# Kernel tuning notes

Hardware: AMD Instinct MI355X
Metric: run time of the kernel (lower is better)

The kernel has to match this reference:

```python
import jax, jax.numpy as jnp
import numpy as np

N = 100_000      # points
F = 64           # feature dim
B = 4            # graphs in batch
POOL_RAD = 0.2   # voxel size
D = 8            # static upper bound on voxels per spatial dim
M_MAX = 1024     # static upper bound on number of nonempty clusters


def setup_inputs() -> dict:
    key = jax.random.key(0)
    k1, k2, k3 = jax.random.split(key, 3)
    pos = jax.random.uniform(k1, (N, 3), dtype=jnp.float32)
    x = jax.random.normal(k2, (N, F), dtype=jnp.float32)
    batch = jnp.sort(jax.random.randint(k3, (N,), 0, B)).astype(jnp.int32)
    return {"pos": pos, "x": x, "batch": batch}


def reference(pos, x, batch):
    batch = batch.astype(jnp.int32)
    rad = jnp.asarray(POOL_RAD, pos.dtype)
    # --- voxel_grid clustering (start = min - rad/2 as in the torch module) ---
    start = pos.min(axis=0) - rad * 0.5
    coords = jnp.clip(jnp.floor((pos - start) / rad).astype(jnp.int32), 0, D - 1)  # [N,3]
    vox = ((batch * D + coords[:, 0]) * D + coords[:, 1]) * D + coords[:, 2]       # [N]
    V = B * D * D * D
    # --- consecutive_cluster + scatter mean of positions ---
    ones = jnp.ones((pos.shape[0],), pos.dtype)
    counts = jax.ops.segment_sum(ones, vox, num_segments=V)       # [V]
    sum_pos = jax.ops.segment_sum(pos, vox, num_segments=V)       # [V,3]
    nonempty = counts > 0
    # compact nonempty voxels to static M_MAX slots (padding duplicates voxel idx 0;
    # argmin tie-breaking to the first index keeps duplicates inert)
    idx = jnp.nonzero(nonempty, size=M_MAX, fill_value=0)[0]      # [M_MAX]
    valid = jnp.arange(M_MAX) < jnp.sum(nonempty)                 # [M_MAX]
    centroids = sum_pos[idx] / jnp.maximum(counts[idx], 1.0)[:, None]  # [M_MAX,3]
    new_batch = idx // (D * D * D)                                # [M_MAX]
    # --- nearest: assign each point to nearest cluster centroid in same graph ---
    d2 = (jnp.sum(pos * pos, axis=1)[:, None]
          - 2.0 * pos @ centroids.T
          + jnp.sum(centroids * centroids, axis=1)[None, :])      # [N, M_MAX]
    big = jnp.asarray(1e30, pos.dtype)
    d2 = jnp.where((batch[:, None] == new_batch[None, :]) & valid[None, :], d2, big)
    assign = jnp.argmin(d2, axis=1)                               # [N]
    # --- scatter max of features into clusters (empty clusters -> 0, as in PyG) ---
    x_pool = jax.ops.segment_max(x, assign, num_segments=M_MAX)   # [M_MAX, F]
    x_pool = jnp.where(jnp.isfinite(x_pool), x_pool, jnp.zeros_like(x_pool))
    return x_pool, centroids, new_batch, valid
```

## Files before the change

kernel.cpp:

```cpp
#include <hip/hip_runtime.h>
#include <stdint.h>

#define DGRID 8
#define NVOX  2048
#define NBATCH 4
#define MMAX  1024
#define FDIM  64
#define CHUNKP 256
#define GRP   20

__device__ __forceinline__ unsigned encf(float f){
  unsigned u = __float_as_uint(f);
  return (u & 0x80000000u) ? ~u : (u | 0x80000000u);
}
__device__ __forceinline__ float decf(unsigned e){
  unsigned u = (e & 0x80000000u) ? (e ^ 0x80000000u) : ~e;
  return __uint_as_float(u);
}


__global__ __launch_bounds__(256) void k_minpart(const float* __restrict__ pos,
    int N, unsigned* __restrict__ bmin){
  unsigned m0 = 0xFFFFFFFFu, m1 = 0xFFFFFFFFu, m2 = 0xFFFFFFFFu;
  int stride = gridDim.x * blockDim.x;
  for (int i = blockIdx.x * blockDim.x + threadIdx.x; i < N; i += stride){
    unsigned e0 = encf(pos[3*i+0]); if (e0 < m0) m0 = e0;
    unsigned e1 = encf(pos[3*i+1]); if (e1 < m1) m1 = e1;
    unsigned e2 = encf(pos[3*i+2]); if (e2 < m2) m2 = e2;
  }
  #pragma unroll
  for (int off = 32; off > 0; off >>= 1){
    unsigned t0 = __shfl_down(m0, off); if (t0 < m0) m0 = t0;
    unsigned t1 = __shfl_down(m1, off); if (t1 < m1) m1 = t1;
    unsigned t2 = __shfl_down(m2, off); if (t2 < m2) m2 = t2;
  }
  __shared__ unsigned sm[4][3];
  int wv = threadIdx.x >> 6, lane = threadIdx.x & 63;
  if (lane == 0){ sm[wv][0] = m0; sm[wv][1] = m1; sm[wv][2] = m2; }
  __syncthreads();
  if (threadIdx.x == 0){
    unsigned a0 = sm[0][0], a1 = sm[0][1], a2 = sm[0][2];
    for (int k = 1; k < 4; k++){
      if (sm[k][0] < a0) a0 = sm[k][0];
      if (sm[k][1] < a1) a1 = sm[k][1];
      if (sm[k][2] < a2) a2 = sm[k][2];
    }
    bmin[blockIdx.x*3+0] = a0;
    bmin[blockIdx.x*3+1] = a1;
    bmin[blockIdx.x*3+2] = a2;
  }
}

__global__ __launch_bounds__(256) void k_vox_hist(const float* __restrict__ pos,
    const int* __restrict__ batch, int N, const unsigned* __restrict__ bmin,
    int* __restrict__ vox, int* __restrict__ chunkHist){
  __shared__ int h[NVOX];
  __shared__ unsigned smin[3];
  for (int t = threadIdx.x; t < NVOX; t += 256) h[t] = 0;
  if (threadIdx.x < 64){
    unsigned a0 = bmin[threadIdx.x*3+0];
    unsigned a1 = bmin[threadIdx.x*3+1];
    unsigned a2 = bmin[threadIdx.x*3+2];
    #pragma unroll
    for (int off = 32; off > 0; off >>= 1){
      unsigned t0 = __shfl_down(a0, off); if (t0 < a0) a0 = t0;
      unsigned t1 = __shfl_down(a1, off); if (t1 < a1) a1 = t1;
      unsigned t2 = __shfl_down(a2, off); if (t2 < a2) a2 = t2;
    }
    if (threadIdx.x == 0){ smin[0] = a0; smin[1] = a1; smin[2] = a2; }
  }
  __syncthreads();
  int c = blockIdx.x;
  int i = c * CHUNKP + threadIdx.x;
  if (i < N){
    float s0 = __fsub_rn(decf(smin[0]), 0.1f);
    float s1 = __fsub_rn(decf(smin[1]), 0.1f);
    float s2 = __fsub_rn(decf(smin[2]), 0.1f);
    float q0 = __fdiv_rn(__fsub_rn(pos[3*i+0], s0), 0.2f);
    float q1 = __fdiv_rn(__fsub_rn(pos[3*i+1], s1), 0.2f);
    float q2 = __fdiv_rn(__fsub_rn(pos[3*i+2], s2), 0.2f);
    int c0 = (int)floorf(q0); c0 = c0 < 0 ? 0 : (c0 > DGRID-1 ? DGRID-1 : c0);
    int c1 = (int)floorf(q1); c1 = c1 < 0 ? 0 : (c1 > DGRID-1 ? DGRID-1 : c1);
    int c2 = (int)floorf(q2); c2 = c2 < 0 ? 0 : (c2 > DGRID-1 ? DGRID-1 : c2);
    int v = ((batch[i]*DGRID + c0)*DGRID + c1)*DGRID + c2;
    vox[i] = v;
    atomicAdd(&h[v], 1);
  }
  __syncthreads();
  for (int t = threadIdx.x; t < NVOX; t += 256)
    chunkHist[c * NVOX + t] = h[t];
}

__global__ __launch_bounds__(256) void k_gsum(int nchunks, int ngroups,
    const int* __restrict__ chunkHist, int* __restrict__ gsum){
  int g = blockIdx.x >> 3;
  int v = (blockIdx.x & 7) * 256 + threadIdx.x;
  if (g >= ngroups) return;
  int c0 = g * GRP, c1 = min(nchunks, c0 + GRP);
  int s = 0;
  for (int c = c0; c < c1; c++) s += chunkHist[c * NVOX + v];
  gsum[g * NVOX + v] = s;
}

__global__ __launch_bounds__(256) void k_gscan(int ngroups,
    int* __restrict__ gsum, int* __restrict__ counts, int* __restrict__ clustCnt){
  if (blockIdx.x < 4) clustCnt[blockIdx.x * 256 + threadIdx.x] = 0;
  int v = blockIdx.x * 256 + threadIdx.x;
  if (v >= NVOX) return;
  int run = 0;
  for (int g = 0; g < ngroups; g++){
    int t = gsum[g * NVOX + v];
    gsum[g * NVOX + v] = run;
    run += t;
  }
  counts[v] = run;
}

__global__ __launch_bounds__(64) void k_scan_fast(const int* __restrict__ counts,
    int* Mout, int* batchStartC, int* __restrict__ idxOfCluster,
    int* __restrict__ voxBase){
  int lane = threadIdx.x;
  int cs[32];
  int ne = 0, tot = 0;
  #pragma unroll
  for (int j = 0; j < 32; j++){
    int c = counts[lane*32 + j];
    cs[j] = c;
    ne += (c > 0) ? 1 : 0;
    tot += c;
  }
  int inc = ne, incT = tot;
  #pragma unroll
  for (int off = 1; off < 64; off <<= 1){
    int t  = __shfl_up(inc,  off);
    int tt = __shfl_up(incT, off);
    if (lane >= off){ inc += t; incT += tt; }
  }
  int exne = inc - ne;
  int bb   = incT - tot;
  int run = exne;
  #pragma unroll
  for (int j = 0; j < 32; j++){
    voxBase[lane*32 + j] = bb;
    bb += cs[j];
    if (cs[j] > 0){
      if (run < MMAX) idxOfCluster[run] = lane*32 + j;
      run++;
    }
  }
  int M = __shfl(run, 63);
  for (int m = M + lane; m < MMAX; m += 64) idxOfCluster[m] = 0;
  int ex0  = __shfl(exne, 0);
  int ex16 = __shfl(exne, 16);
  int ex32 = __shfl(exne, 32);
  int ex48 = __shfl(exne, 48);
  if (lane == 0){
    Mout[0] = M;
    batchStartC[0] = ex0;  batchStartC[1] = ex16;
    batchStartC[2] = ex32; batchStartC[3] = ex48;
    batchStartC[NBATCH] = (M < MMAX) ? M : MMAX;
  }
}

__global__ __launch_bounds__(256) void k_scatter(const float* __restrict__ pos,
    const int* __restrict__ vox, int N, const int* __restrict__ chunkHist,
    const int* __restrict__ gsum, const int* __restrict__ voxBase,
    float* __restrict__ pos_sorted){
  __shared__ int base[NVOX];
  __shared__ int rowCnt[4][NVOX];
  int c = blockIdx.x;
  int g = c / GRP, cg0 = g * GRP;
  for (int t = threadIdx.x; t < NVOX; t += 256){
    int b = voxBase[t] + gsum[g * NVOX + t];
    for (int cc = cg0; cc < c; cc++) b += chunkHist[cc * NVOX + t];
    base[t] = b;
    rowCnt[0][t] = 0; rowCnt[1][t] = 0; rowCnt[2][t] = 0; rowCnt[3][t] = 0;
  }
  __syncthreads();
  int r = threadIdx.x >> 6;
  int lane = threadIdx.x & 63;
  int i = c * CHUNKP + r*64 + lane;
  bool valid = i < N;
  int v = valid ? vox[i] : -1;
  float px = 0.f, py = 0.f, pz = 0.f;
  if (valid){ px = pos[3*i+0]; py = pos[3*i+1]; pz = pos[3*i+2]; }
  int rank = 0, cnt = 0;
  #pragma unroll 8
  for (int j = 0; j < 64; j++){
    int vj = __shfl(v, j);
    if (vj == v){
      cnt++;
      if (j < lane) rank++;
    }
  }
  if (valid && rank == 0) rowCnt[r][v] = cnt;
  __syncthreads();
  if (valid){
    int pre = 0;
    for (int rr = 0; rr < r; rr++) pre += rowCnt[rr][v];
    int dst = base[v] + pre + rank;
    pos_sorted[3*dst+0] = px;
    pos_sorted[3*dst+1] = py;
    pos_sorted[3*dst+2] = pz;
  }
}

__global__ __launch_bounds__(64) void k_sum2cent(const float* __restrict__ pos_sorted,
    const int* __restrict__ voxBase, const int* __restrict__ counts,
    float4* __restrict__ centv){
  int v = blockIdx.x * 64 + threadIdx.x;
  if (v >= NVOX) return;
  int lo = voxBase[v], cnt = counts[v];
  const float* p = pos_sorted + 3*(size_t)lo;
  float sx = 0.f, sy = 0.f, sz = 0.f;
  int k = 0;
  for (; k + 4 <= cnt; k += 4){
    float a0 = p[0],  a1 = p[1],  a2 = p[2];
    float b0 = p[3],  b1 = p[4],  b2 = p[5];
    float c0 = p[6],  c1 = p[7],  c2 = p[8];
    float d0 = p[9],  d1 = p[10], d2 = p[11];
    sx = __fadd_rn(__fadd_rn(__fadd_rn(__fadd_rn(sx, a0), b0), c0), d0);
    sy = __fadd_rn(__fadd_rn(__fadd_rn(__fadd_rn(sy, a1), b1), c1), d1);
    sz = __fadd_rn(__fadd_rn(__fadd_rn(__fadd_rn(sz, a2), b2), c2), d2);
    p += 12;
  }
  for (; k < cnt; k++){
    sx = __fadd_rn(sx, p[0]);
    sy = __fadd_rn(sy, p[1]);
    sz = __fadd_rn(sz, p[2]);
    p += 3;
  }
  float den = fmaxf((float)cnt, 1.0f);
  float cx = __fdiv_rn(sx, den);
  float cy = __fdiv_rn(sy, den);
  float cz = __fdiv_rn(sz, den);
  float c2 = __fadd_rn(__fadd_rn(__fmul_rn(cx,cx), __fmul_rn(cy,cy)), __fmul_rn(cz,cz));
  centv[v] = make_float4(cx, cy, cz, c2);
}

__global__ __launch_bounds__(256) void k_argmin2(const float* __restrict__ pos,
    const int* __restrict__ batch, int N, const float4* __restrict__ centv,
    const int* __restrict__ idxOfCluster, const int* __restrict__ Mout,
    const int* __restrict__ batchStartC, int* __restrict__ assign,
    int* __restrict__ clustCnt, float* __restrict__ outC,
    float* __restrict__ outNB, float* __restrict__ outValid){
  __shared__ float4 sc[MMAX];
  __shared__ int h[MMAX];
  for (int m = threadIdx.x; m < MMAX; m += 256){
    sc[m] = centv[idxOfCluster[m]];
    h[m] = 0;
  }
  __syncthreads();
  if (blockIdx.x == 0){
    int M = Mout[0];
    for (int m = threadIdx.x; m < MMAX; m += 256){
      float4 cc = sc[m];
      outC[3*m+0] = cc.x; outC[3*m+1] = cc.y; outC[3*m+2] = cc.z;
      outNB[m] = (float)(idxOfCluster[m] >> 9);
      outValid[m] = (m < M) ? 1.0f : 0.0f;
    }
  }
  int i = blockIdx.x * 256 + threadIdx.x;
  if (i < N){
    float px = pos[3*i+0], py = pos[3*i+1], pz = pos[3*i+2];
    float p2 = __fadd_rn(__fadd_rn(__fmul_rn(px,px), __fmul_rn(py,py)), __fmul_rn(pz,pz));
    int b = batch[i];
    int mlo = batchStartC[b], mhi = batchStartC[b+1];
    float best = 3.402823466e+38f;
    int bm = mlo;
    for (int m = mlo; m < mhi; m++){
      float4 cc = sc[m];
      float dot = __fadd_rn(__fadd_rn(__fmul_rn(px,cc.x), __fmul_rn(py,cc.y)),
                            __fmul_rn(pz,cc.z));
      float d2  = __fadd_rn(__fsub_rn(p2, __fmul_rn(2.0f, dot)), cc.w);
      if (d2 < best){ best = d2; bm = m; }
    }
    assign[i] = bm;
    atomicAdd(&h[bm], 1);
  }
  __syncthreads();
  for (int t = threadIdx.x; t < MMAX; t += 256){
    int c = h[t];
    if (c > 0) atomicAdd(&clustCnt[t], c);
  }
}

__global__ __launch_bounds__(64) void k_cbase2(const int* __restrict__ clustCnt,
    int* __restrict__ clustBase, int* __restrict__ cur){
  int lane = threadIdx.x;
  int cs[16]; int tot = 0;
  #pragma unroll
  for (int j = 0; j < 16; j++){ cs[j] = clustCnt[lane*16 + j]; tot += cs[j]; }
  int inc = tot;
  #pragma unroll
  for (int off = 1; off < 64; off <<= 1){
    int t = __shfl_up(inc, off);
    if (lane >= off) inc += t;
  }
  int bb = inc - tot;
  #pragma unroll
  for (int j = 0; j < 16; j++){
    clustBase[lane*16 + j] = bb;
    cur[lane*16 + j] = bb;
    bb += cs[j];
  }
}

__global__ __launch_bounds__(256) void k_scatter2s(const int* __restrict__ assign,
    int N, int* __restrict__ cur, int* __restrict__ idx_sorted){
  int i = blockIdx.x * 256 + threadIdx.x;
  if (i >= N) return;
  int m = assign[i];
  int p = atomicAdd(&cur[m], 1);
  idx_sorted[p] = i;
}

__global__ __launch_bounds__(256) void k_xmax(const float* __restrict__ x,
    const int* __restrict__ idx_sorted, const int* __restrict__ clustBase,
    const int* __restrict__ clustCnt, float* __restrict__ outX){
  int w = blockIdx.x * 4 + (threadIdx.x >> 6);
  int lane = threadIdx.x & 63;
  if (w >= MMAX) return;
  int lo = clustBase[w], cnt = clustCnt[w];
  float mx = -3.402823466e+38f;
  int k = 0;
  for (; k + 4 <= cnt; k += 4){
    int r0 = idx_sorted[lo+k+0], r1 = idx_sorted[lo+k+1];
    int r2 = idx_sorted[lo+k+2], r3 = idx_sorted[lo+k+3];
    float a = x[(size_t)r0 * FDIM + lane];
    float b = x[(size_t)r1 * FDIM + lane];
    float c = x[(size_t)r2 * FDIM + lane];
    float d = x[(size_t)r3 * FDIM + lane];
    mx = fmaxf(mx, fmaxf(fmaxf(a, b), fmaxf(c, d)));
  }
  for (; k < cnt; k++){
    int r0 = idx_sorted[lo+k];
    mx = fmaxf(mx, x[(size_t)r0 * FDIM + lane]);
  }
  outX[w * FDIM + lane] = (cnt > 0) ? mx : 0.0f;
}


__global__ __launch_bounds__(256) void k_init(unsigned* startEnc, int* batchCnt){
  int t = threadIdx.x;
  if (t < 3) startEnc[t] = 0xFFFFFFFFu;
  if (t < NBATCH) batchCnt[t] = 0;
}

__global__ __launch_bounds__(256) void k_min_hist(const float* __restrict__ pos,
    const int* __restrict__ batch, int N, unsigned* startEnc, int* batchCnt){
  __shared__ int sbin[NBATCH];
  if (threadIdx.x < NBATCH) sbin[threadIdx.x] = 0;
  __syncthreads();
  unsigned m0 = 0xFFFFFFFFu, m1 = 0xFFFFFFFFu, m2 = 0xFFFFFFFFu;
  int stride = gridDim.x * blockDim.x;
  for (int i = blockIdx.x * blockDim.x + threadIdx.x; i < N; i += stride){
    unsigned e0 = encf(pos[3*i+0]); if (e0 < m0) m0 = e0;
    unsigned e1 = encf(pos[3*i+1]); if (e1 < m1) m1 = e1;
    unsigned e2 = encf(pos[3*i+2]); if (e2 < m2) m2 = e2;
    atomicAdd(&sbin[batch[i]], 1);
  }
  #pragma unroll
  for (int off = 32; off > 0; off >>= 1){
    unsigned t0 = __shfl_down(m0, off); if (t0 < m0) m0 = t0;
    unsigned t1 = __shfl_down(m1, off); if (t1 < m1) m1 = t1;
    unsigned t2 = __shfl_down(m2, off); if (t2 < m2) m2 = t2;
  }
  if ((threadIdx.x & 63) == 0){
    atomicMin(&startEnc[0], m0);
    atomicMin(&startEnc[1], m1);
    atomicMin(&startEnc[2], m2);
  }
  __syncthreads();
  if (threadIdx.x < NBATCH) atomicAdd(&batchCnt[threadIdx.x], sbin[threadIdx.x]);
}

__global__ __launch_bounds__(256) void k_vox(const float* __restrict__ pos,
    const int* __restrict__ batch, int N, const unsigned* __restrict__ startEnc,
    int* __restrict__ vox, int* __restrict__ counts){
  int i = blockIdx.x * blockDim.x + threadIdx.x;
  if (i >= N) return;
  float s0 = __fsub_rn(decf(startEnc[0]), 0.1f);
  float s1 = __fsub_rn(decf(startEnc[1]), 0.1f);
  float s2 = __fsub_rn(decf(startEnc[2]), 0.1f);
  float q0 = __fdiv_rn(__fsub_rn(pos[3*i+0], s0), 0.2f);
  float q1 = __fdiv_rn(__fsub_rn(pos[3*i+1], s1), 0.2f);
  float q2 = __fdiv_rn(__fsub_rn(pos[3*i+2], s2), 0.2f);
  int c0 = (int)floorf(q0); c0 = c0 < 0 ? 0 : (c0 > DGRID-1 ? DGRID-1 : c0);
  int c1 = (int)floorf(q1); c1 = c1 < 0 ? 0 : (c1 > DGRID-1 ? DGRID-1 : c1);
  int c2 = (int)floorf(q2); c2 = c2 < 0 ? 0 : (c2 > DGRID-1 ? DGRID-1 : c2);
  int v = ((batch[i]*DGRID + c0)*DGRID + c1)*DGRID + c2;
  vox[i] = v;
  atomicAdd(&counts[v], 1);
}

__global__ __launch_bounds__(64) void k_scan_old(const int* __restrict__ counts,
    const int* __restrict__ batchCnt, int* batchPtr, int* Mout,
    int* batchStartC, int* __restrict__ idxOfCluster, int* __restrict__ voxBase){
  int lane = threadIdx.x;
  int cs[32];
  int ne = 0, tot = 0;
  #pragma unroll
  for (int j = 0; j < 32; j++){
    int c = counts[lane*32 + j];
    cs[j] = c;
    ne += (c > 0) ? 1 : 0;
    tot += c;
  }
  int inc = ne, incT = tot;
  #pragma unroll
  for (int off = 1; off < 64; off <<= 1){
    int t  = __shfl_up(inc,  off);
    int tt = __shfl_up(incT, off);
    if (lane >= off){ inc += t; incT += tt; }
  }
  int exne = inc - ne;
  int bb   = incT - tot;
  int run = exne;
  #pragma unroll
  for (int j = 0; j < 32; j++){
    voxBase[lane*32 + j] = bb;
    bb += cs[j];
    if (cs[j] > 0){
      if (run < MMAX) idxOfCluster[run] = lane*32 + j;
      run++;
    }
  }
  int M = __shfl(run, 63);
  for (int m = M + lane; m < MMAX; m += 64) idxOfCluster[m] = 0;
  int ex0  = __shfl(exne, 0);
  int ex16 = __shfl(exne, 16);
  int ex32 = __shfl(exne, 32);
  int ex48 = __shfl(exne, 48);
  if (lane == 0){
    Mout[0] = M;
    int acc = 0;
    for (int b = 0; b < NBATCH; b++){ batchPtr[b] = acc; acc += batchCnt[b]; }
    batchPtr[NBATCH] = acc;
    batchStartC[0] = ex0;  batchStartC[1] = ex16;
    batchStartC[2] = ex32; batchStartC[3] = ex48;
    batchStartC[NBATCH] = (M < MMAX) ? M : MMAX;
  }
}

__global__ __launch_bounds__(64) void k_sum(const float* __restrict__ pos,
    const int* __restrict__ vox, const int* __restrict__ counts,
    const int* __restrict__ batchPtr, float* __restrict__ sum_pos){
  int v = blockIdx.x * 64 + threadIdx.x;
  if (v >= NVOX) return;
  int b = v >> 9;
  int lo = batchPtr[b], hi = batchPtr[b+1];
  float sx = 0.f, sy = 0.f, sz = 0.f;
  if (counts[v] > 0){
    for (int i = lo; i < hi; i++){
      if (vox[i] == v){
        sx = __fadd_rn(sx, pos[3*i+0]);
        sy = __fadd_rn(sy, pos[3*i+1]);
        sz = __fadd_rn(sz, pos[3*i+2]);
      }
    }
  }
  sum_pos[3*v+0] = sx;
  sum_pos[3*v+1] = sy;
  sum_pos[3*v+2] = sz;
}

__global__ __launch_bounds__(256) void k_cent(const float* __restrict__ sum_pos,
    const int* __restrict__ counts, const int* __restrict__ idxOfCluster,
    const int* __restrict__ Mout, float4* __restrict__ cent4,
    float* __restrict__ outC, float* __restrict__ outNB, float* __restrict__ outValid){
  int m = blockIdx.x * blockDim.x + threadIdx.x;
  if (m >= MMAX) return;
  int M = Mout[0];
  int v = idxOfCluster[m];
  float den = fmaxf((float)counts[v], 1.0f);
  float cx = __fdiv_rn(sum_pos[3*v+0], den);
  float cy = __fdiv_rn(sum_pos[3*v+1], den);
  float cz = __fdiv_rn(sum_pos[3*v+2], den);
  float c2 = __fadd_rn(__fadd_rn(__fmul_rn(cx,cx), __fmul_rn(cy,cy)), __fmul_rn(cz,cz));
  cent4[m] = make_float4(cx, cy, cz, c2);
  outC[3*m+0] = cx; outC[3*m+1] = cy; outC[3*m+2] = cz;
  outNB[m] = (float)(v >> 9);
  outValid[m] = (m < M) ? 1.0f : 0.0f;
}

__global__ __launch_bounds__(256) void k_assign_slow(const float* __restrict__ pos,
    const float* __restrict__ x, const int* __restrict__ batch, int N,
    const float4* __restrict__ cent4, const int* __restrict__ batchStartC,
    unsigned* __restrict__ encMax){
  __shared__ float4 sc[MMAX];
  for (int m = threadIdx.x; m < MMAX; m += blockDim.x) sc[m] = cent4[m];
  __syncthreads();
  int i = blockIdx.x * blockDim.x + threadIdx.x;
  if (i >= N) return;
  float px = pos[3*i+0], py = pos[3*i+1], pz = pos[3*i+2];
  float p2 = __fadd_rn(__fadd_rn(__fmul_rn(px,px), __fmul_rn(py,py)), __fmul_rn(pz,pz));
  int b = batch[i];
  int mlo = batchStartC[b], mhi = batchStartC[b+1];
  float best = 3.402823466e+38f;
  int bm = mlo;
  for (int m = mlo; m < mhi; m++){
    float4 c = sc[m];
    float dot = __fadd_rn(__fadd_rn(__fmul_rn(px,c.x), __fmul_rn(py,c.y)),
                          __fmul_rn(pz,c.z));
    float d2  = __fadd_rn(__fsub_rn(p2, __fmul_rn(2.0f, dot)), c.w);
    if (d2 < best){ best = d2; bm = m; }
  }
  unsigned* dst = encMax + bm * FDIM;
  const float4* xi = (const float4*)(x + (size_t)i * FDIM);
  #pragma unroll
  for (int f4 = 0; f4 < FDIM/4; f4++){
    float4 xv = xi[f4];
    atomicMax(&dst[4*f4+0], encf(xv.x));
    atomicMax(&dst[4*f4+1], encf(xv.y));
    atomicMax(&dst[4*f4+2], encf(xv.z));
    atomicMax(&dst[4*f4+3], encf(xv.w));
  }
}
__global__ __launch_bounds__(256) void k_decode(const unsigned* __restrict__ encMax,
    float* __restrict__ outX){
  int t = blockIdx.x * blockDim.x + threadIdx.x;
  if (t >= MMAX * FDIM) return;
  unsigned e = encMax[t];
  outX[t] = (e == 0u) ? 0.0f : decf(e);
}


extern "C" void kernel_launch(void* const* d_in, const int* in_sizes, int n_in,
                              void* d_out, int out_size, void* d_ws, size_t ws_size,
                              hipStream_t stream){
  const float* pos   = (const float*)d_in[0];
  const float* x     = (const float*)d_in[1];
  const int*   batch = (const int*)d_in[2];
  const int N = in_sizes[2];

  char* w = (char*)d_ws;
  unsigned* bmin         = (unsigned*)(w + 0);
  unsigned* startEnc     = (unsigned*)(w + 768);
  int*      batchCnt     = (int*)(w + 784);
  int*      batchPtr     = (int*)(w + 800);
  int*      Mout         = (int*)(w + 832);
  int*      batchStartC  = (int*)(w + 848);
  int*      counts       = (int*)(w + 896);
  int*      voxBase      = (int*)(w + 9088);
  float*    sum_pos      = (float*)(w + 17280);
  int*      idxOfCluster = (int*)(w + 41856);
  float4*   cent4        = (float4*)(w + 45952);
  int*      clustCnt     = (int*)(w + 62336);
  int*      clustBase    = (int*)(w + 66432);
  int*      cur          = (int*)(w + 70528);
  float4*   centv        = (float4*)(w + 74624);
  unsigned* encMax       = (unsigned*)(w + 107392);
  int*      gsum         = (int*)(w + 107392);
  int*      vox          = (int*)(w + 369536);
  size_t voxEnd = 369536 + (size_t)N * 4;
  size_t chOff  = (voxEnd + 15) & ~(size_t)15;

  int nchunks = (N + CHUNKP - 1) / CHUNKP;
  int ngroups = (nchunks + GRP - 1) / GRP;
  size_t psOff = chOff + (size_t)nchunks * NVOX * 4;
  size_t need  = psOff + (size_t)N * 3 * 4;
  const bool fast = (ws_size >= need) && (ngroups <= 32);

  int*   chunkHist  = (int*)(w + chOff);
  float* pos_sorted = (float*)(w + psOff);
  int* assign     = (int*)pos_sorted;
  int* idx_sorted = (int*)pos_sorted + N;

  float* outX     = (float*)d_out;
  float* outC     = outX + MMAX * FDIM;
  float* outNB    = outC + MMAX * 3;
  float* outValid = outNB + MMAX;

  const int nb = (N + 255) / 256;
  if (fast){
    k_minpart<<<64, 256, 0, stream>>>(pos, N, bmin);
    k_vox_hist<<<nchunks, 256, 0, stream>>>(pos, batch, N, bmin, vox, chunkHist);
    k_gsum<<<ngroups * 8, 256, 0, stream>>>(nchunks, ngroups, chunkHist, gsum);
    k_gscan<<<NVOX / 256, 256, 0, stream>>>(ngroups, gsum, counts, clustCnt);
    k_scan_fast<<<1, 64, 0, stream>>>(counts, Mout, batchStartC, idxOfCluster, voxBase);
    k_scatter<<<nchunks, 256, 0, stream>>>(pos, vox, N, chunkHist, gsum, voxBase,
                                           pos_sorted);
    k_sum2cent<<<NVOX / 64, 64, 0, stream>>>(pos_sorted, voxBase, counts, centv);
    k_argmin2<<<nb, 256, 0, stream>>>(pos, batch, N, centv, idxOfCluster, Mout,
                                      batchStartC, assign, clustCnt,
                                      outC, outNB, outValid);
    k_cbase2<<<1, 64, 0, stream>>>(clustCnt, clustBase, cur);
    k_scatter2s<<<nb, 256, 0, stream>>>(assign, N, cur, idx_sorted);
    k_xmax<<<MMAX / 4, 256, 0, stream>>>(x, idx_sorted, clustBase, clustCnt, outX);
  } else {
    k_init<<<1, 256, 0, stream>>>(startEnc, batchCnt);
    hipMemsetAsync(counts, 0, NVOX * 4, stream);
    hipMemsetAsync(encMax, 0, MMAX * FDIM * 4, stream);
    k_min_hist<<<256, 256, 0, stream>>>(pos, batch, N, startEnc, batchCnt);
    k_vox<<<nb, 256, 0, stream>>>(pos, batch, N, startEnc, vox, counts);
    k_scan_old<<<1, 64, 0, stream>>>(counts, batchCnt, batchPtr, Mout, batchStartC,
                                     idxOfCluster, voxBase);
    k_sum<<<(NVOX + 63) / 64, 64, 0, stream>>>(pos, vox, counts, batchPtr, sum_pos);
    k_cent<<<MMAX / 256, 256, 0, stream>>>(sum_pos, counts, idxOfCluster, Mout,
                                           cent4, outC, outNB, outValid);
    k_assign_slow<<<nb, 256, 0, stream>>>(pos, x, batch, N, cent4, batchStartC, encMax);
    k_decode<<<(MMAX * FDIM + 255) / 256, 256, 0, stream>>>(encMax, outX);
  }
}
```

Measured before the change: 154.1 us.

## Replace chunked histogram and counting-sort pipeline with global atomics and wave-ballot sums

Drops the per-chunk histogram, group prefix sums and position scatter into voxel-sorted order. Voxel counts now come from global atomics, and each wave builds one voxel's centroid by scanning that batch's point range with ballot and summing matching points in index order, which keeps the summation order deterministic. Zeroing of the count buffers moves into the min-reduction kernel. This removes several launches and the chunkHist and pos_sorted traffic, but each voxel's wave rescans its whole batch segment of vox (about 25k points), which adds a lot of redundant reads, and it adds contention on the global atomics.

```diff
diff --git a/kernel.cpp b/kernel.cpp
--- a/kernel.cpp
+++ b/kernel.cpp
@@ -6,8 +6,6 @@
 #define NBATCH 4
 #define MMAX  1024
 #define FDIM  64
-#define CHUNKP 256
-#define GRP   20
 
 __device__ __forceinline__ unsigned encf(float f){
   unsigned u = __float_as_uint(f);
@@ -20,7 +18,10 @@
 
 
 __global__ __launch_bounds__(256) void k_minpart(const float* __restrict__ pos,
-    int N, unsigned* __restrict__ bmin){
+    int N, unsigned* __restrict__ bmin, int* __restrict__ counts,
+    int* __restrict__ clustCnt){
+  if (blockIdx.x < 8) counts[blockIdx.x * 256 + threadIdx.x] = 0;
+  else if (blockIdx.x < 12) clustCnt[(blockIdx.x - 8) * 256 + threadIdx.x] = 0;
   unsigned m0 = 0xFFFFFFFFu, m1 = 0xFFFFFFFFu, m2 = 0xFFFFFFFFu;
   int stride = gridDim.x * blockDim.x;
   for (int i = blockIdx.x * blockDim.x + threadIdx.x; i < N; i += stride){
@@ -51,12 +52,10 @@
   }
 }
 
-__global__ __launch_bounds__(256) void k_vox_hist(const float* __restrict__ pos,
+__global__ __launch_bounds__(256) void k_voxcnt(const float* __restrict__ pos,
     const int* __restrict__ batch, int N, const unsigned* __restrict__ bmin,
-    int* __restrict__ vox, int* __restrict__ chunkHist){
-  __shared__ int h[NVOX];
+    int* __restrict__ vox, int* __restrict__ counts){
   __shared__ unsigned smin[3];
-  for (int t = threadIdx.x; t < NVOX; t += 256) h[t] = 0;
   if (threadIdx.x < 64){
     unsigned a0 = bmin[threadIdx.x*3+0];
     unsigned a1 = bmin[threadIdx.x*3+1];
@@ -70,55 +69,24 @@
     if (threadIdx.x == 0){ smin[0] = a0; smin[1] = a1; smin[2] = a2; }
   }
   __syncthreads();
-  int c = blockIdx.x;
-  int i = c * CHUNKP + threadIdx.x;
-  if (i < N){
-    float s0 = __fsub_rn(decf(smin[0]), 0.1f);
-    float s1 = __fsub_rn(decf(smin[1]), 0.1f);
-    float s2 = __fsub_rn(decf(smin[2]), 0.1f);
-    float q0 = __fdiv_rn(__fsub_rn(pos[3*i+0], s0), 0.2f);
-    float q1 = __fdiv_rn(__fsub_rn(pos[3*i+1], s1), 0.2f);
-    float q2 = __fdiv_rn(__fsub_rn(pos[3*i+2], s2), 0.2f);
-    int c0 = (int)floorf(q0); c0 = c0 < 0 ? 0 : (c0 > DGRID-1 ? DGRID-1 : c0);
-    int c1 = (int)floorf(q1); c1 = c1 < 0 ? 0 : (c1 > DGRID-1 ? DGRID-1 : c1);
-    int c2 = (int)floorf(q2); c2 = c2 < 0 ? 0 : (c2 > DGRID-1 ? DGRID-1 : c2);
-    int v = ((batch[i]*DGRID + c0)*DGRID + c1)*DGRID + c2;
-    vox[i] = v;
-    atomicAdd(&h[v], 1);
-  }
-  __syncthreads();
-  for (int t = threadIdx.x; t < NVOX; t += 256)
-    chunkHist[c * NVOX + t] = h[t];
-}
-
-__global__ __launch_bounds__(256) void k_gsum(int nchunks, int ngroups,
-    const int* __restrict__ chunkHist, int* __restrict__ gsum){
-  int g = blockIdx.x >> 3;
-  int v = (blockIdx.x & 7) * 256 + threadIdx.x;
-  if (g >= ngroups) return;
-  int c0 = g * GRP, c1 = min(nchunks, c0 + GRP);
-  int s = 0;
-  for (int c = c0; c < c1; c++) s += chunkHist[c * NVOX + v];
-  gsum[g * NVOX + v] = s;
-}
-
-__global__ __launch_bounds__(256) void k_gscan(int ngroups,
-    int* __restrict__ gsum, int* __restrict__ counts, int* __restrict__ clustCnt){
-  if (blockIdx.x < 4) clustCnt[blockIdx.x * 256 + threadIdx.x] = 0;
-  int v = blockIdx.x * 256 + threadIdx.x;
-  if (v >= NVOX) return;
-  int run = 0;
-  for (int g = 0; g < ngroups; g++){
-    int t = gsum[g * NVOX + v];
-    gsum[g * NVOX + v] = run;
-    run += t;
-  }
-  counts[v] = run;
+  int i = blockIdx.x * 256 + threadIdx.x;
+  if (i >= N) return;
+  float s0 = __fsub_rn(decf(smin[0]), 0.1f);
+  float s1 = __fsub_rn(decf(smin[1]), 0.1f);
+  float s2 = __fsub_rn(decf(smin[2]), 0.1f);
+  float q0 = __fdiv_rn(__fsub_rn(pos[3*i+0], s0), 0.2f);
+  float q1 = __fdiv_rn(__fsub_rn(pos[3*i+1], s1), 0.2f);
+  float q2 = __fdiv_rn(__fsub_rn(pos[3*i+2], s2), 0.2f);
+  int c0 = (int)floorf(q0); c0 = c0 < 0 ? 0 : (c0 > DGRID-1 ? DGRID-1 : c0);
+  int c1 = (int)floorf(q1); c1 = c1 < 0 ? 0 : (c1 > DGRID-1 ? DGRID-1 : c1);
+  int c2 = (int)floorf(q2); c2 = c2 < 0 ? 0 : (c2 > DGRID-1 ? DGRID-1 : c2);
+  int v = ((batch[i]*DGRID + c0)*DGRID + c1)*DGRID + c2;
+  vox[i] = v;
+  atomicAdd(&counts[v], 1);
 }
 
 __global__ __launch_bounds__(64) void k_scan_fast(const int* __restrict__ counts,
-    int* Mout, int* batchStartC, int* __restrict__ idxOfCluster,
-    int* __restrict__ voxBase){
+    int* Mout, int* batchStartC, int* batchPtr, int* __restrict__ idxOfCluster){
   int lane = threadIdx.x;
   int cs[32];
   int ne = 0, tot = 0;
@@ -137,12 +105,10 @@
     if (lane >= off){ inc += t; incT += tt; }
   }
   int exne = inc - ne;
-  int bb   = incT - tot;
+  int exT  = incT - tot;
   int run = exne;
   #pragma unroll
   for (int j = 0; j < 32; j++){
-    voxBase[lane*32 + j] = bb;
-    bb += cs[j];
     if (cs[j] > 0){
       if (run < MMAX) idxOfCluster[run] = lane*32 + j;
       run++;
@@ -150,92 +116,58 @@
   }
   int M = __shfl(run, 63);
   for (int m = M + lane; m < MMAX; m += 64) idxOfCluster[m] = 0;
-  int ex0  = __shfl(exne, 0);
-  int ex16 = __shfl(exne, 16);
-  int ex32 = __shfl(exne, 32);
-  int ex48 = __shfl(exne, 48);
+  int ex0  = __shfl(exne, 0),  ex16 = __shfl(exne, 16);
+  int ex32 = __shfl(exne, 32), ex48 = __shfl(exne, 48);
+  int t0 = __shfl(exT, 0),  t16 = __shfl(exT, 16);
+  int t32 = __shfl(exT, 32), t48 = __shfl(exT, 48);
+  int tN = __shfl(incT, 63);
   if (lane == 0){
     Mout[0] = M;
     batchStartC[0] = ex0;  batchStartC[1] = ex16;
     batchStartC[2] = ex32; batchStartC[3] = ex48;
     batchStartC[NBATCH] = (M < MMAX) ? M : MMAX;
-  }
-}
-
-__global__ __launch_bounds__(256) void k_scatter(const float* __restrict__ pos,
-    const int* __restrict__ vox, int N, const int* __restrict__ chunkHist,
-    const int* __restrict__ gsum, const int* __restrict__ voxBase,
-    float* __restrict__ pos_sorted){
-  __shared__ int base[NVOX];
-  __shared__ int rowCnt[4][NVOX];
-  int c = blockIdx.x;
-  int g = c / GRP, cg0 = g * GRP;
-  for (int t = threadIdx.x; t < NVOX; t += 256){
-    int b = voxBase[t] + gsum[g * NVOX + t];
-    for (int cc = cg0; cc < c; cc++) b += chunkHist[cc * NVOX + t];
-    base[t] = b;
-    rowCnt[0][t] = 0; rowCnt[1][t] = 0; rowCnt[2][t] = 0; rowCnt[3][t] = 0;
-  }
-  __syncthreads();
-  int r = threadIdx.x >> 6;
+    batchPtr[0] = t0;  batchPtr[1] = t16;
+    batchPtr[2] = t32; batchPtr[3] = t48;
+    batchPtr[4] = tN;
+  }
+}
+
+__global__ __launch_bounds__(256) void k_wavesum(const float* __restrict__ pos,
+    const int* __restrict__ vox, const int* __restrict__ counts,
+    const int* __restrict__ batchPtr, float4* __restrict__ centv){
+  int v = blockIdx.x * 4 + (threadIdx.x >> 6);
   int lane = threadIdx.x & 63;
-  int i = c * CHUNKP + r*64 + lane;
-  bool valid = i < N;
-  int v = valid ? vox[i] : -1;
-  float px = 0.f, py = 0.f, pz = 0.f;
-  if (valid){ px = pos[3*i+0]; py = pos[3*i+1]; pz = pos[3*i+2]; }
-  int rank = 0, cnt = 0;
-  #pragma unroll 8
-  for (int j = 0; j < 64; j++){
-    int vj = __shfl(v, j);
-    if (vj == v){
-      cnt++;
-      if (j < lane) rank++;
-    }
-  }
-  if (valid && rank == 0) rowCnt[r][v] = cnt;
-  __syncthreads();
-  if (valid){
-    int pre = 0;
-    for (int rr = 0; rr < r; rr++) pre += rowCnt[rr][v];
-    int dst = base[v] + pre + rank;
-    pos_sorted[3*dst+0] = px;
-    pos_sorted[3*dst+1] = py;
-    pos_sorted[3*dst+2] = pz;
-  }
-}
-
-__global__ __launch_bounds__(64) void k_sum2cent(const float* __restrict__ pos_sorted,
-    const int* __restrict__ voxBase, const int* __restrict__ counts,
-    float4* __restrict__ centv){
-  int v = blockIdx.x * 64 + threadIdx.x;
   if (v >= NVOX) return;
-  int lo = voxBase[v], cnt = counts[v];
-  const float* p = pos_sorted + 3*(size_t)lo;
+  int cnt = counts[v];
   float sx = 0.f, sy = 0.f, sz = 0.f;
-  int k = 0;
-  for (; k + 4 <= cnt; k += 4){
-    float a0 = p[0],  a1 = p[1],  a2 = p[2];
-    float b0 = p[3],  b1 = p[4],  b2 = p[5];
-    float c0 = p[6],  c1 = p[7],  c2 = p[8];
-    float d0 = p[9],  d1 = p[10], d2 = p[11];
-    sx = __fadd_rn(__fadd_rn(__fadd_rn(__fadd_rn(sx, a0), b0), c0), d0);
-    sy = __fadd_rn(__fadd_rn(__fadd_rn(__fadd_rn(sy, a1), b1), c1), d1);
-    sz = __fadd_rn(__fadd_rn(__fadd_rn(__fadd_rn(sz, a2), b2), c2), d2);
-    p += 12;
-  }
-  for (; k < cnt; k++){
-    sx = __fadd_rn(sx, p[0]);
-    sy = __fadd_rn(sy, p[1]);
-    sz = __fadd_rn(sz, p[2]);
-    p += 3;
-  }
-  float den = fmaxf((float)cnt, 1.0f);
-  float cx = __fdiv_rn(sx, den);
-  float cy = __fdiv_rn(sy, den);
-  float cz = __fdiv_rn(sz, den);
-  float c2 = __fadd_rn(__fadd_rn(__fmul_rn(cx,cx), __fmul_rn(cy,cy)), __fmul_rn(cz,cz));
-  centv[v] = make_float4(cx, cy, cz, c2);
+  if (cnt > 0){
+    int b = v >> 9;
+    int lo = batchPtr[b], hi = batchPtr[b+1];
+    int found = 0;
+    for (int base = lo; base < hi && found < cnt; base += 64){
+      int i = base + lane;
+      int vi = (i < hi) ? vox[i] : -1;
+      unsigned long long mask = __ballot(vi == v);
+      found += __popcll(mask);
+      while (mask){
+        int j = __ffsll((unsigned long long)mask) - 1;
+        mask &= mask - 1;
+        int idx = base + j;
+        sx = __fadd_rn(sx, pos[3*idx+0]);
+        sy = __fadd_rn(sy, pos[3*idx+1]);
+        sz = __fadd_rn(sz, pos[3*idx+2]);
+      }
+    }
+  }
+  if (lane == 0){
+    float den = fmaxf((float)cnt, 1.0f);
+    float cx = __fdiv_rn(sx, den);
+    float cy = __fdiv_rn(sy, den);
+    float cz = __fdiv_rn(sz, den);
+    float c2 = __fadd_rn(__fadd_rn(__fmul_rn(cx,cx), __fmul_rn(cy,cy)),
+                         __fmul_rn(cz,cz));
+    centv[v] = make_float4(cx, cy, cz, c2);
+  }
 }
 
 __global__ __launch_bounds__(256) void k_argmin2(const float* __restrict__ pos,
@@ -551,21 +483,12 @@
   int*      cur          = (int*)(w + 70528);
   float4*   centv        = (float4*)(w + 74624);
   unsigned* encMax       = (unsigned*)(w + 107392);
-  int*      gsum         = (int*)(w + 107392);
   int*      vox          = (int*)(w + 369536);
-  size_t voxEnd = 369536 + (size_t)N * 4;
-  size_t chOff  = (voxEnd + 15) & ~(size_t)15;
-
-  int nchunks = (N + CHUNKP - 1) / CHUNKP;
-  int ngroups = (nchunks + GRP - 1) / GRP;
-  size_t psOff = chOff + (size_t)nchunks * NVOX * 4;
-  size_t need  = psOff + (size_t)N * 3 * 4;
-  const bool fast = (ws_size >= need) && (ngroups <= 32);
-
-  int*   chunkHist  = (int*)(w + chOff);
-  float* pos_sorted = (float*)(w + psOff);
-  int* assign     = (int*)pos_sorted;
-  int* idx_sorted = (int*)pos_sorted + N;
+  size_t aOff = 369536 + (size_t)N * 4;
+  int*      assign       = (int*)(w + aOff);
+  int*      idx_sorted   = (int*)(w + aOff) + N;
+  size_t need = aOff + (size_t)N * 8;
+  const bool fast = (ws_size >= need);
 
   float* outX     = (float*)d_out;
   float* outC     = outX + MMAX * FDIM;
@@ -574,14 +497,11 @@
 
   const int nb = (N + 255) / 256;
   if (fast){
-    k_minpart<<<64, 256, 0, stream>>>(pos, N, bmin);
-    k_vox_hist<<<nchunks, 256, 0, stream>>>(pos, batch, N, bmin, vox, chunkHist);
-    k_gsum<<<ngroups * 8, 256, 0, stream>>>(nchunks, ngroups, chunkHist, gsum);
-    k_gscan<<<NVOX / 256, 256, 0, stream>>>(ngroups, gsum, counts, clustCnt);
-    k_scan_fast<<<1, 64, 0, stream>>>(counts, Mout, batchStartC, idxOfCluster, voxBase);
-    k_scatter<<<nchunks, 256, 0, stream>>>(pos, vox, N, chunkHist, gsum, voxBase,
-                                           pos_sorted);
-    k_sum2cent<<<NVOX / 64, 64, 0, stream>>>(pos_sorted, voxBase, counts, centv);
+    k_minpart<<<64, 256, 0, stream>>>(pos, N, bmin, counts, clustCnt);
+    k_voxcnt<<<nb, 256, 0, stream>>>(pos, batch, N, bmin, vox, counts);
+    k_scan_fast<<<1, 64, 0, stream>>>(counts, Mout, batchStartC, batchPtr,
+                                      idxOfCluster);
+    k_wavesum<<<NVOX / 4, 256, 0, stream>>>(pos, vox, counts, batchPtr, centv);
     k_argmin2<<<nb, 256, 0, stream>>>(pos, batch, N, centv, idxOfCluster, Mout,
                                       batchStartC, assign, clustCnt,
                                       outC, outNB, outValid);
```

Measured after the change: 229.3 us. 1.49x slower.

## Fold single-wave scan kernels into scatter kernels to cut launches

Applied to the files above, without the earlier changes.

Removes the two single-block scan kernels (voxel scan and cluster-base scan) by having every block of the following scatter kernel redo the small prefix scan in its first wave, with block 0 writing the global results. Zeroing of counters moves into the first kernel, and the cluster scatter uses a separate rank counter plus the per-block computed base instead of a pre-initialized cursor array. This trades two kernel launches and their serialization gaps for redundant per-block scan work and extra global reads of counts.

```diff
diff --git a/kernel.cpp b/kernel.cpp
--- a/kernel.cpp
+++ b/kernel.cpp
@@ -20,7 +20,11 @@
 
 
 __global__ __launch_bounds__(256) void k_minpart(const float* __restrict__ pos,
-    int N, unsigned* __restrict__ bmin){
+    int N, unsigned* __restrict__ bmin, int* __restrict__ counts,
+    int* __restrict__ clustCnt, int* __restrict__ clustRank){
+  if (blockIdx.x < 8) counts[blockIdx.x * 256 + threadIdx.x] = 0;
+  else if (blockIdx.x < 12) clustCnt[(blockIdx.x - 8) * 256 + threadIdx.x] = 0;
+  else if (blockIdx.x < 16) clustRank[(blockIdx.x - 12) * 256 + threadIdx.x] = 0;
   unsigned m0 = 0xFFFFFFFFu, m1 = 0xFFFFFFFFu, m2 = 0xFFFFFFFFu;
   int stride = gridDim.x * blockDim.x;
   for (int i = blockIdx.x * blockDim.x + threadIdx.x; i < N; i += stride){
@@ -103,8 +107,7 @@
 }
 
 __global__ __launch_bounds__(256) void k_gscan(int ngroups,
-    int* __restrict__ gsum, int* __restrict__ counts, int* __restrict__ clustCnt){
-  if (blockIdx.x < 4) clustCnt[blockIdx.x * 256 + threadIdx.x] = 0;
+    int* __restrict__ gsum, int* __restrict__ counts){
   int v = blockIdx.x * 256 + threadIdx.x;
   if (v >= NVOX) return;
   int run = 0;
@@ -116,70 +119,69 @@
   counts[v] = run;
 }
 
-__global__ __launch_bounds__(64) void k_scan_fast(const int* __restrict__ counts,
-    int* Mout, int* batchStartC, int* __restrict__ idxOfCluster,
-    int* __restrict__ voxBase){
-  int lane = threadIdx.x;
-  int cs[32];
-  int ne = 0, tot = 0;
-  #pragma unroll
-  for (int j = 0; j < 32; j++){
-    int c = counts[lane*32 + j];
-    cs[j] = c;
-    ne += (c > 0) ? 1 : 0;
-    tot += c;
-  }
-  int inc = ne, incT = tot;
-  #pragma unroll
-  for (int off = 1; off < 64; off <<= 1){
-    int t  = __shfl_up(inc,  off);
-    int tt = __shfl_up(incT, off);
-    if (lane >= off){ inc += t; incT += tt; }
-  }
-  int exne = inc - ne;
-  int bb   = incT - tot;
-  int run = exne;
-  #pragma unroll
-  for (int j = 0; j < 32; j++){
-    voxBase[lane*32 + j] = bb;
-    bb += cs[j];
-    if (cs[j] > 0){
-      if (run < MMAX) idxOfCluster[run] = lane*32 + j;
-      run++;
-    }
-  }
-  int M = __shfl(run, 63);
-  for (int m = M + lane; m < MMAX; m += 64) idxOfCluster[m] = 0;
-  int ex0  = __shfl(exne, 0);
-  int ex16 = __shfl(exne, 16);
-  int ex32 = __shfl(exne, 32);
-  int ex48 = __shfl(exne, 48);
-  if (lane == 0){
-    Mout[0] = M;
-    batchStartC[0] = ex0;  batchStartC[1] = ex16;
-    batchStartC[2] = ex32; batchStartC[3] = ex48;
-    batchStartC[NBATCH] = (M < MMAX) ? M : MMAX;
-  }
-}
-
 __global__ __launch_bounds__(256) void k_scatter(const float* __restrict__ pos,
     const int* __restrict__ vox, int N, const int* __restrict__ chunkHist,
-    const int* __restrict__ gsum, const int* __restrict__ voxBase,
-    float* __restrict__ pos_sorted){
-  __shared__ int base[NVOX];
+    const int* __restrict__ gsum, const int* __restrict__ counts,
+    int* Mout, int* batchStartC, int* __restrict__ idxOfCluster,
+    int* __restrict__ voxBaseG, float* __restrict__ pos_sorted){
+  __shared__ int sBase[NVOX];
   __shared__ int rowCnt[4][NVOX];
   int c = blockIdx.x;
-  int g = c / GRP, cg0 = g * GRP;
-  for (int t = threadIdx.x; t < NVOX; t += 256){
-    int b = voxBase[t] + gsum[g * NVOX + t];
-    for (int cc = cg0; cc < c; cc++) b += chunkHist[cc * NVOX + t];
-    base[t] = b;
-    rowCnt[0][t] = 0; rowCnt[1][t] = 0; rowCnt[2][t] = 0; rowCnt[3][t] = 0;
-  }
-  __syncthreads();
-  int r = threadIdx.x >> 6;
-  int lane = threadIdx.x & 63;
-  int i = c * CHUNKP + r*64 + lane;
+  int wv = threadIdx.x >> 6, lane = threadIdx.x & 63;
+  if (wv == 0){
+    int cs[32];
+    int ne = 0, tot = 0;
+    #pragma unroll
+    for (int j = 0; j < 32; j++){
+      int cc2 = counts[lane*32 + j];
+      cs[j] = cc2; ne += (cc2 > 0) ? 1 : 0; tot += cc2;
+    }
+    int inc = ne, incT = tot;
+    #pragma unroll
+    for (int off = 1; off < 64; off <<= 1){
+      int t  = __shfl_up(inc,  off);
+      int tt = __shfl_up(incT, off);
+      if (lane >= off){ inc += t; incT += tt; }
+    }
+    int exne = inc - ne, exT = incT - tot;
+    int run = exne, bb = exT;
+    #pragma unroll
+    for (int j = 0; j < 32; j++){
+      sBase[lane*32 + j] = bb;
+      if (c == 0) voxBaseG[lane*32 + j] = bb;
+      bb += cs[j];
+      if (cs[j] > 0){
+        if (c == 0 && run < MMAX) idxOfCluster[run] = lane*32 + j;
+        run++;
+      }
+    }
+    if (c == 0){
+      int M = __shfl(run, 63);
+      for (int m = M + lane; m < MMAX; m += 64) idxOfCluster[m] = 0;
+      int ex0  = __shfl(exne, 0),  ex16 = __shfl(exne, 16);
+      int ex32 = __shfl(exne, 32), ex48 = __shfl(exne, 48);
+      if (lane == 0){
+        Mout[0] = M;
+        batchStartC[0] = ex0;  batchStartC[1] = ex16;
+        batchStartC[2] = ex32; batchStartC[3] = ex48;
+        batchStartC[NBATCH] = (M < MMAX) ? M : MMAX;
+      }
+    }
+  } else {
+    for (int t = threadIdx.x - 64; t < 4*NVOX; t += 192)
+      ((int*)rowCnt)[t] = 0;
+  }
+  __syncthreads();
+  {
+    int g = c / GRP, cg0 = g * GRP;
+    for (int t = threadIdx.x; t < NVOX; t += 256){
+      int b = sBase[t] + gsum[g * NVOX + t];
+      for (int cc = cg0; cc < c; cc++) b += chunkHist[cc * NVOX + t];
+      sBase[t] = b;
+    }
+  }
+  __syncthreads();
+  int i = c * CHUNKP + threadIdx.x;
   bool valid = i < N;
   int v = valid ? vox[i] : -1;
   float px = 0.f, py = 0.f, pz = 0.f;
@@ -193,12 +195,12 @@
       if (j < lane) rank++;
     }
   }
-  if (valid && rank == 0) rowCnt[r][v] = cnt;
+  if (valid && rank == 0) rowCnt[wv][v] = cnt;
   __syncthreads();
   if (valid){
     int pre = 0;
-    for (int rr = 0; rr < r; rr++) pre += rowCnt[rr][v];
-    int dst = base[v] + pre + rank;
+    for (int rr = 0; rr < wv; rr++) pre += rowCnt[rr][v];
+    int dst = sBase[v] + pre + rank;
     pos_sorted[3*dst+0] = px;
     pos_sorted[3*dst+1] = py;
     pos_sorted[3*dst+2] = pz;
@@ -285,34 +287,35 @@
   }
 }
 
-__global__ __launch_bounds__(64) void k_cbase2(const int* __restrict__ clustCnt,
-    int* __restrict__ clustBase, int* __restrict__ cur){
-  int lane = threadIdx.x;
-  int cs[16]; int tot = 0;
-  #pragma unroll
-  for (int j = 0; j < 16; j++){ cs[j] = clustCnt[lane*16 + j]; tot += cs[j]; }
-  int inc = tot;
-  #pragma unroll
-  for (int off = 1; off < 64; off <<= 1){
-    int t = __shfl_up(inc, off);
-    if (lane >= off) inc += t;
-  }
-  int bb = inc - tot;
-  #pragma unroll
-  for (int j = 0; j < 16; j++){
-    clustBase[lane*16 + j] = bb;
-    cur[lane*16 + j] = bb;
-    bb += cs[j];
-  }
-}
-
 __global__ __launch_bounds__(256) void k_scatter2s(const int* __restrict__ assign,
-    int N, int* __restrict__ cur, int* __restrict__ idx_sorted){
+    int N, const int* __restrict__ clustCnt, int* __restrict__ clustRank,
+    int* __restrict__ clustBaseG, int* __restrict__ idx_sorted){
+  __shared__ int cb[MMAX];
+  int wv = threadIdx.x >> 6, lane = threadIdx.x & 63;
+  if (wv == 0){
+    int cs[16]; int tot = 0;
+    #pragma unroll
+    for (int j = 0; j < 16; j++){ cs[j] = clustCnt[lane*16 + j]; tot += cs[j]; }
+    int inc = tot;
+    #pragma unroll
+    for (int off = 1; off < 64; off <<= 1){
+      int t = __shfl_up(inc, off);
+      if (lane >= off) inc += t;
+    }
+    int bb = inc - tot;
+    #pragma unroll
+    for (int j = 0; j < 16; j++){
+      cb[lane*16 + j] = bb;
+      if (blockIdx.x == 0) clustBaseG[lane*16 + j] = bb;
+      bb += cs[j];
+    }
+  }
+  __syncthreads();
   int i = blockIdx.x * 256 + threadIdx.x;
   if (i >= N) return;
   int m = assign[i];
-  int p = atomicAdd(&cur[m], 1);
-  idx_sorted[p] = i;
+  int r = atomicAdd(&clustRank[m], 1);
+  idx_sorted[cb[m] + r] = i;
 }
 
 __global__ __launch_bounds__(256) void k_xmax(const float* __restrict__ x,
@@ -542,13 +545,13 @@
   int*      Mout         = (int*)(w + 832);
   int*      batchStartC  = (int*)(w + 848);
   int*      counts       = (int*)(w + 896);
-  int*      voxBase      = (int*)(w + 9088);
+  int*      voxBaseG     = (int*)(w + 9088);
   float*    sum_pos      = (float*)(w + 17280);
   int*      idxOfCluster = (int*)(w + 41856);
   float4*   cent4        = (float4*)(w + 45952);
   int*      clustCnt     = (int*)(w + 62336);
-  int*      clustBase    = (int*)(w + 66432);
-  int*      cur          = (int*)(w + 70528);
+  int*      clustBaseG   = (int*)(w + 66432);
+  int*      clustRank    = (int*)(w + 70528);
   float4*   centv        = (float4*)(w + 74624);
   unsigned* encMax       = (unsigned*)(w + 107392);
   int*      gsum         = (int*)(w + 107392);
@@ -574,20 +577,20 @@
 
   const int nb = (N + 255) / 256;
   if (fast){
-    k_minpart<<<64, 256, 0, stream>>>(pos, N, bmin);
+    k_minpart<<<64, 256, 0, stream>>>(pos, N, bmin, counts, clustCnt, clustRank);
     k_vox_hist<<<nchunks, 256, 0, stream>>>(pos, batch, N, bmin, vox, chunkHist);
     k_gsum<<<ngroups * 8, 256, 0, stream>>>(nchunks, ngroups, chunkHist, gsum);
-    k_gscan<<<NVOX / 256, 256, 0, stream>>>(ngroups, gsum, counts, clustCnt);
-    k_scan_fast<<<1, 64, 0, stream>>>(counts, Mout, batchStartC, idxOfCluster, voxBase);
-    k_scatter<<<nchunks, 256, 0, stream>>>(pos, vox, N, chunkHist, gsum, voxBase,
-                                           pos_sorted);
-    k_sum2cent<<<NVOX / 64, 64, 0, stream>>>(pos_sorted, voxBase, counts, centv);
+    k_gscan<<<NVOX / 256, 256, 0, stream>>>(ngroups, gsum, counts);
+    k_scatter<<<nchunks, 256, 0, stream>>>(pos, vox, N, chunkHist, gsum, counts,
+                                           Mout, batchStartC, idxOfCluster,
+                                           voxBaseG, pos_sorted);
+    k_sum2cent<<<NVOX / 64, 64, 0, stream>>>(pos_sorted, voxBaseG, counts, centv);
     k_argmin2<<<nb, 256, 0, stream>>>(pos, batch, N, centv, idxOfCluster, Mout,
                                       batchStartC, assign, clustCnt,
                                       outC, outNB, outValid);
-    k_cbase2<<<1, 64, 0, stream>>>(clustCnt, clustBase, cur);
-    k_scatter2s<<<nb, 256, 0, stream>>>(assign, N, cur, idx_sorted);
-    k_xmax<<<MMAX / 4, 256, 0, stream>>>(x, idx_sorted, clustBase, clustCnt, outX);
+    k_scatter2s<<<nb, 256, 0, stream>>>(assign, N, clustCnt, clustRank,
+                                        clustBaseG, idx_sorted);
+    k_xmax<<<MMAX / 4, 256, 0, stream>>>(x, idx_sorted, clustBaseG, clustCnt, outX);
   } else {
     k_init<<<1, 256, 0, stream>>>(startEnc, batchCnt);
     hipMemsetAsync(counts, 0, NVOX * 4, stream);
@@ -595,7 +598,7 @@
     k_min_hist<<<256, 256, 0, stream>>>(pos, batch, N, startEnc, batchCnt);
     k_vox<<<nb, 256, 0, stream>>>(pos, batch, N, startEnc, vox, counts);
     k_scan_old<<<1, 64, 0, stream>>>(counts, batchCnt, batchPtr, Mout, batchStartC,
-                                     idxOfCluster, voxBase);
+                                     idxOfCluster, voxBaseG);
     k_sum<<<(NVOX + 63) / 64, 64, 0, stream>>>(pos, vox, counts, batchPtr, sum_pos);
     k_cent<<<MMAX / 256, 256, 0, stream>>>(sum_pos, counts, idxOfCluster, Mout,
                                            cent4, outC, outNB, outValid);
```

Measured after the change: 149.6 us, median of 2. 1.03x faster.
